# Kernel tuning notes

Hardware: AMD Instinct MI355X
Metric: run time of the kernel (lower is better)

The kernel has to match this reference:

```python
import jax, jax.numpy as jnp
import numpy as np

N_NODES = 10000
DEG = 16
E = N_NODES * DEG
IN = 256
OUT = 256
B = 2
SLOPE = 0.2


def setup_inputs() -> dict:
    key = jax.random.key(0)
    ks = jax.random.split(key, 8)
    rng = np.random.default_rng(0)
    # edges sorted by source, every node appears as a source exactly DEG times
    src = np.repeat(np.arange(N_NODES, dtype=np.int64), DEG)
    tgt = rng.integers(0, N_NODES, size=E).astype(np.int64)
    # torch.unique(..., return_inverse=True) -> sorted uniques + inverse ids
    usrc, sid = np.unique(src, return_inverse=True)
    utgt, tid = np.unique(tgt, return_inverse=True)
    s = 1.0 / np.sqrt(IN)
    sa = 1.0 / np.sqrt(2 * OUT)
    return {
        "nodes": jax.random.normal(ks[0], (N_NODES, B, IN), jnp.float32),
        "Ws": jax.random.normal(ks[1], (IN, OUT), jnp.float32) * s,
        "bs": jnp.zeros((OUT,), jnp.float32),
        "Wt": jax.random.normal(ks[2], (IN, OUT), jnp.float32) * s,
        "bt": jnp.zeros((OUT,), jnp.float32),
        "Wv": jax.random.normal(ks[3], (IN, OUT), jnp.float32) * s,
        "bv": jnp.zeros((OUT,), jnp.float32),
        "Wa": jax.random.normal(ks[4], (2 * OUT, 1), jnp.float32) * sa,
        "ba": jnp.zeros((1,), jnp.float32),
        "unique_source_node_id": jnp.asarray(usrc),
        "unique_target_node_id": jnp.asarray(utgt),
        "source_id_per_edge": jnp.asarray(sid),
        "target_id_per_edge": jnp.asarray(tid),
    }


def reference(nodes, Ws, bs, Wt, bt, Wv, bv, Wa, ba,
              unique_source_node_id, unique_target_node_id,
              source_id_per_edge, target_id_per_edge):
    Ns = unique_source_node_id.shape[0]
    # project_node_states
    src_proj = nodes[unique_source_node_id] @ Ws + bs          # [Ns, B, O]
    tgt_proj = nodes[unique_target_node_id] @ Wt + bt          # [Nt, B, O]
    # gather_node_pairs + attention + LeakyReLU
    paired = jnp.concatenate(
        [src_proj[source_id_per_edge], tgt_proj[target_id_per_edge]], axis=-1)  # [E, B, 2O]
    scores = jax.nn.leaky_relu(paired @ Wa + ba, SLOPE)        # [E, B, 1]
    # neighbourhood_softmax: exp(clip) then scatter-add over source segments
    ex = jnp.exp(jnp.clip(scores, -2.0, 2.0))
    denom = jax.ops.segment_sum(ex, source_id_per_edge, num_segments=Ns)
    alpha = ex / denom[source_id_per_edge]                     # [E, B, 1]
    # apply_attention (values_type='new')
    vals = nodes[unique_target_node_id] @ Wv + bv              # [Nt, B, O]
    weighted = alpha * vals[target_id_per_edge]                # [E, B, O]
    # aggregate_neighbours: the original indexes the per-edge weighted values
    # by target_id_per_edge along the EDGE axis (faithfully reproduced), then
    # sums contiguous same-source segments.
    gathered = weighted[target_id_per_edge]                    # [E, B, O]
    agg = jax.ops.segment_sum(gathered, source_id_per_edge, num_segments=Ns)
    # update_sources (update_type='sum'), return_only_source_nodes=True
    return src_proj + agg                                      # [Ns, B, O]
```

## Files before the change

kernel.cpp:

```cpp
#include <hip/hip_runtime.h>

#define B2 2
#define DEG 16
#define SLOPE 0.2f

typedef __attribute__((ext_vector_type(8))) short short8;
typedef __attribute__((ext_vector_type(8))) unsigned short ushort8;
typedef __attribute__((ext_vector_type(4))) unsigned short ushort4v;
typedef __attribute__((ext_vector_type(4))) float f32x4;

__device__ inline unsigned short f2bf(float f) {
  union { float f; unsigned u; } v; v.f = f;
  unsigned r = v.u + 0x7fff + ((v.u >> 16) & 1);
  return (unsigned short)(r >> 16);
}
__device__ inline float bf2f(unsigned short u) {
  union { unsigned u; float f; } c; c.u = ((unsigned)u) << 16;
  return c.f;
}
__device__ inline ushort8 f2bf8(float4 lo, float4 hi) {
  ushort8 r;
  r[0] = f2bf(lo.x); r[1] = f2bf(lo.y); r[2] = f2bf(lo.z); r[3] = f2bf(lo.w);
  r[4] = f2bf(hi.x); r[5] = f2bf(hi.y); r[6] = f2bf(hi.z); r[7] = f2bf(hi.w);
  return r;
}

__device__ inline float wave_dot256(const float* __restrict__ a,
                                    const float* __restrict__ b, int lane) {
  float4 x = *(const float4*)(a + lane * 4);
  float4 y = *(const float4*)(b + lane * 4);
  float v = x.x * y.x + x.y * y.y + x.z * y.z + x.w * y.w;
  #pragma unroll
  for (int off = 32; off; off >>= 1) v += __shfl_down(v, off);
  return v;
}

__global__ __launch_bounds__(256) void prep_w_k(
    const float* __restrict__ Ws, const float* __restrict__ Wt,
    const float* __restrict__ Wv, const float* __restrict__ Wa,
    const float* __restrict__ bs, const float* __restrict__ bt,
    unsigned short* __restrict__ WsT, unsigned short* __restrict__ WvT,
    float* __restrict__ ws_comb, float* __restrict__ wt_comb,
    float* __restrict__ consts) {
  int bx = blockIdx.x;
  if (bx < 32) {
    const float* src = (bx & 16) ? Wv : Ws;
    unsigned short* dst = (bx & 16) ? WvT : WsT;
    int rc = bx & 15;
    int r0 = (rc >> 2) * 64, c0 = (rc & 3) * 64;
    __shared__ float tile[64][65];
    int tr = threadIdx.x >> 6, tc = threadIdx.x & 63;
    #pragma unroll
    for (int i = 0; i < 16; ++i) {
      int r = tr * 16 + i;
      tile[r][tc] = src[(long)(r0 + r) * 256 + c0 + tc];
    }
    __syncthreads();
    #pragma unroll
    for (int i = 0; i < 16; ++i) {
      int r = tr * 16 + i;
      dst[(long)(c0 + r) * 256 + r0 + tc] = f2bf(tile[tc][r]);
    }
  } else {
    int wave = (bx - 32) * 4 + (threadIdx.x >> 6);
    int lane = threadIdx.x & 63;
    if (wave >= 514) return;
    const float *vec, *wa;
    float* dst;
    if (wave < 256)       { vec = Ws + (long)wave * 256;         wa = Wa;       dst = ws_comb + wave; }
    else if (wave < 512)  { vec = Wt + (long)(wave - 256) * 256; wa = Wa + 256; dst = wt_comb + (wave - 256); }
    else if (wave == 512) { vec = bs; wa = Wa;       dst = consts; }
    else                  { vec = bt; wa = Wa + 256; dst = consts + 1; }
    float v = wave_dot256(vec, wa, lane);
    if (lane == 0) *dst = v;
  }
}

__global__ __launch_bounds__(256) void logits_k(
    const float* __restrict__ nodes, const float* __restrict__ ws_comb,
    const float* __restrict__ wt_comb,
    float* __restrict__ an_s, float* __restrict__ an_t, int nrows) {
  int wave = blockIdx.x * 4 + (threadIdx.x >> 6);
  int lane = threadIdx.x & 63;
  if (wave >= nrows) return;
  const float4 a = *(const float4*)(nodes + (long)wave * 256 + lane * 4);
  const float4 w1 = *(const float4*)(ws_comb + lane * 4);
  const float4 w2 = *(const float4*)(wt_comb + lane * 4);
  float vs = a.x * w1.x + a.y * w1.y + a.z * w1.z + a.w * w1.w;
  float vt = a.x * w2.x + a.y * w2.y + a.z * w2.z + a.w * w2.w;
  #pragma unroll
  for (int off = 32; off; off >>= 1) {
    vs += __shfl_down(vs, off);
    vt += __shfl_down(vt, off);
  }
  if (lane == 0) { an_s[wave] = vs; an_t[wave] = vt; }
}

__global__ __launch_bounds__(256, 2) void gemm_mfma_k(
    const float* __restrict__ nodesf,
    const int* __restrict__ usrc, const int* __restrict__ utgt,
    const unsigned short* __restrict__ WsT, const unsigned short* __restrict__ WvT,
    const float* __restrict__ bs, const float* __restrict__ bv,
    unsigned short* __restrict__ sproj_bf, unsigned short* __restrict__ vals_bf,
    const float* __restrict__ an_s, const float* __restrict__ an_t,
    const int* __restrict__ tid_arr, const float* __restrict__ consts,
    const float* __restrict__ ba, float* __restrict__ alpha,
    int Ms, int Mt, int Ns) {
  if (blockIdx.z == 2) {
    if (blockIdx.y != 0) return;
    int g = blockIdx.x * 256 + threadIdx.x;
    int s = g >> 1, b = g & 1;
    if (s >= Ns) return;
    float base = an_s[(long)usrc[s] * B2 + b] + consts[0] + consts[1] + ba[0];
    float ex[DEG];
    float den = 0.f;
    #pragma unroll
    for (int j = 0; j < DEG; ++j) {
      int t = tid_arr[s * DEG + j];
      float sc = base + an_t[(long)utgt[t] * B2 + b];
      sc = sc > 0.f ? sc : SLOPE * sc;
      sc = fminf(2.f, fmaxf(-2.f, sc));
      float ev = __expf(sc);
      ex[j] = ev;
      den += ev;
    }
    float inv = 1.f / den;
    #pragma unroll
    for (int j = 0; j < DEG; ++j) alpha[(long)(s * DEG + j) * B2 + b] = ex[j] * inv;
    return;
  }
  bool second = blockIdx.z != 0;
  const int* idx = second ? utgt : usrc;
  const unsigned short* WT = second ? WvT : WsT;
  const float* bias = second ? bv : bs;
  unsigned short* dstC = second ? vals_bf : sproj_bf;
  int M = second ? Mt : Ms;
  int row0 = blockIdx.x * 128, col0 = blockIdx.y * 128;
  if (row0 >= M) return;

  constexpr int LDT = 72;
  __shared__ unsigned short As[128 * LDT];
  __shared__ unsigned short Bs[128 * LDT];
  int t = threadIdx.x;
  int wv = t >> 6, lane = t & 63;
  int srow = t >> 3;
  int scol = (t & 7) * 8;
  const float* ap[4];
  #pragma unroll
  for (int p = 0; p < 4; ++p) {
    int m = row0 + srow + 32 * p;
    int mc = m < M ? m : M - 1;
    long ar = (long)idx[mc >> 1] * B2 + (mc & 1);
    ap[p] = nodesf + ar * 256 + scol;
  }
  const unsigned short* bp[4];
  #pragma unroll
  for (int q = 0; q < 4; ++q)
    bp[q] = WT + (long)(col0 + srow + 32 * q) * 256 + scol;

  f32x4 acc[2][8];
  #pragma unroll
  for (int i = 0; i < 2; ++i)
    #pragma unroll
    for (int j = 0; j < 8; ++j) acc[i][j] = (f32x4)(0.f);

  float4 af[4][2];
  ushort8 bvv[4];
  #pragma unroll
  for (int p = 0; p < 4; ++p) {
    af[p][0] = *(const float4*)(ap[p]);
    af[p][1] = *(const float4*)(ap[p] + 4);
  }
  #pragma unroll
  for (int q = 0; q < 4; ++q) bvv[q] = *(const ushort8*)(bp[q]);

  #pragma unroll
  for (int k0 = 0; k0 < 256; k0 += 64) {
    __syncthreads();
    #pragma unroll
    for (int p = 0; p < 4; ++p)
      *(ushort8*)&As[(srow + 32 * p) * LDT + scol] = f2bf8(af[p][0], af[p][1]);
    #pragma unroll
    for (int q = 0; q < 4; ++q)
      *(ushort8*)&Bs[(srow + 32 * q) * LDT + scol] = bvv[q];
    __syncthreads();
    if (k0 < 192) {
      #pragma unroll
      for (int p = 0; p < 4; ++p) {
        af[p][0] = *(const float4*)(ap[p] + k0 + 64);
        af[p][1] = *(const float4*)(ap[p] + k0 + 68);
      }
      #pragma unroll
      for (int q = 0; q < 4; ++q) bvv[q] = *(const ushort8*)(bp[q] + k0 + 64);
    }
    #pragma unroll
    for (int ks = 0; ks < 64; ks += 32) {
      int ko = ks + (lane >> 4) * 8;
      short8 af0 = *(const short8*)&As[(32 * wv + (lane & 15)) * LDT + ko];
      short8 af1 = *(const short8*)&As[(32 * wv + 16 + (lane & 15)) * LDT + ko];
      #pragma unroll
      for (int j = 0; j < 8; ++j) {
        short8 bf = *(const short8*)&Bs[(16 * j + (lane & 15)) * LDT + ko];
        acc[0][j] = __builtin_amdgcn_mfma_f32_16x16x32_bf16(bf, af0, acc[0][j], 0, 0, 0);
        acc[1][j] = __builtin_amdgcn_mfma_f32_16x16x32_bf16(bf, af1, acc[1][j], 0, 0, 0);
      }
    }
  }
  int cq = lane >> 4, rl = lane & 15;
  #pragma unroll
  for (int j = 0; j < 8; ++j) {
    int col = col0 + 16 * j + 4 * cq;
    float4 b4 = *(const float4*)(bias + col);
    #pragma unroll
    for (int i = 0; i < 2; ++i) {
      int row = row0 + 32 * wv + 16 * i + rl;
      if (row < M) {
        ushort4v p;
        p[0] = f2bf(acc[i][j][0] + b4.x);
        p[1] = f2bf(acc[i][j][1] + b4.y);
        p[2] = f2bf(acc[i][j][2] + b4.z);
        p[3] = f2bf(acc[i][j][3] + b4.w);
        *(ushort4v*)(dstC + (long)row * 256 + col) = p;
      }
    }
  }
}

__global__ __launch_bounds__(256) void aggregate_k(
    const unsigned short* __restrict__ sproj, const unsigned short* __restrict__ vals,
    const float* __restrict__ alpha, const int* __restrict__ tid_arr,
    float* __restrict__ out, int Ns) {
  int s = blockIdx.x * 4 + (threadIdx.x >> 6);
  int lane = threadIdx.x & 63;
  if (s >= Ns) return;
  int f = tid_arr[s * DEG + (lane & 15)];
  int b = lane >> 5;
  float al = alpha[(long)f * B2 + b];
  int t2 = tid_arr[f];
  ushort8 sp = __builtin_nontemporal_load(
      (const ushort8*)(sproj + (long)s * 512 + lane * 8));
  float acc[8];
  #pragma unroll
  for (int k = 0; k < 8; ++k) acc[k] = bf2f(sp[k]);
  #pragma unroll
  for (int j = 0; j < DEG; ++j) {
    int rr = __shfl(t2, j);
    float aj = __shfl(al, (lane & 32) + j);
    ushort8 v = *(const ushort8*)(vals + (long)rr * 512 + lane * 8);
    #pragma unroll
    for (int k = 0; k < 8; ++k) acc[k] += aj * bf2f(v[k]);
  }
  long ob = (long)s * 512 + lane * 8;
  f32x4 p0, p1;
  p0[0] = acc[0]; p0[1] = acc[1]; p0[2] = acc[2]; p0[3] = acc[3];
  p1[0] = acc[4]; p1[1] = acc[5]; p1[2] = acc[6]; p1[3] = acc[7];
  __builtin_nontemporal_store(p0, (f32x4*)(out + ob));
  __builtin_nontemporal_store(p1, (f32x4*)(out + ob + 4));
}

extern "C" void kernel_launch(void* const* d_in, const int* in_sizes, int n_in,
                              void* d_out, int out_size, void* d_ws, size_t ws_size,
                              hipStream_t stream) {
  const float* nodes = (const float*)d_in[0];
  const float* Ws = (const float*)d_in[1];
  const float* bs = (const float*)d_in[2];
  const float* Wt = (const float*)d_in[3];
  const float* bt = (const float*)d_in[4];
  const float* Wv = (const float*)d_in[5];
  const float* bv = (const float*)d_in[6];
  const float* Wa = (const float*)d_in[7];
  const float* ba = (const float*)d_in[8];
  const int* usrc = (const int*)d_in[9];
  const int* utgt = (const int*)d_in[10];
  const int* tidp = (const int*)d_in[12];
  int Ns = in_sizes[9], Nt = in_sizes[10];
  int NsB = Ns * B2, NtB = Nt * B2;
  long nrows = in_sizes[0] / 256;

  unsigned short* WsT = (unsigned short*)d_ws;
  unsigned short* WvT = WsT + 65536;
  unsigned short* vals_bf = WvT + 65536;
  unsigned short* sproj_bf = vals_bf + (size_t)NtB * 256;
  float* fbase = (float*)(sproj_bf + (size_t)NsB * 256);
  float* an_s = fbase;
  float* an_t = an_s + nrows;
  float* ws_comb = an_t + nrows;
  float* wt_comb = ws_comb + 256;
  float* consts = wt_comb + 256;
  float* alpha = consts + 16;
  float* out = (float*)d_out;

  prep_w_k<<<161, 256, 0, stream>>>(Ws, Wt, Wv, Wa, bs, bt,
                                    WsT, WvT, ws_comb, wt_comb, consts);
  logits_k<<<(int)((nrows + 3) / 4), 256, 0, stream>>>(
      nodes, ws_comb, wt_comb, an_s, an_t, (int)nrows);
  int maxM = NsB > NtB ? NsB : NtB;
  gemm_mfma_k<<<dim3((maxM + 127) / 128, 2, 3), 256, 0, stream>>>(
      nodes, usrc, utgt, WsT, WvT, bs, bv, sproj_bf, vals_bf,
      an_s, an_t, tidp, consts, ba, alpha, NsB, NtB, Ns);
  aggregate_k<<<(Ns + 3) / 4, 256, 0, stream>>>(
      sproj_bf, vals_bf, alpha, tidp, out, Ns);
}
```

Baseline: 133.9 us.

## Fuse attention logits into GEMM A-loads and widen GEMM tile to full N

Removes the separate logits kernel by computing the per-row dot products with the combined attention vectors while the GEMM streams its A rows, reducing them with lane shuffles. The GEMM block now covers all 256 output columns, so each gathered node row is read and converted once instead of twice. Alpha computation moves into its own small kernel that runs after the GEMM, since it now depends on the GEMM's logits. This doubles the accumulator and B-tile shared memory per block, which raises register and LDS pressure and halves the grid size.

```diff
diff --git a/kernel.cpp b/kernel.cpp
--- a/kernel.cpp
+++ b/kernel.cpp
@@ -23,6 +23,10 @@
   r[0] = f2bf(lo.x); r[1] = f2bf(lo.y); r[2] = f2bf(lo.z); r[3] = f2bf(lo.w);
   r[4] = f2bf(hi.x); r[5] = f2bf(hi.y); r[6] = f2bf(hi.z); r[7] = f2bf(hi.w);
   return r;
+}
+__device__ inline float dot8(float4 a0, float4 a1, float4 c0, float4 c1) {
+  return a0.x * c0.x + a0.y * c0.y + a0.z * c0.z + a0.w * c0.w +
+         a1.x * c1.x + a1.y * c1.y + a1.z * c1.z + a1.w * c1.w;
 }
 
 __device__ inline float wave_dot256(const float* __restrict__ a,
@@ -76,71 +80,29 @@
   }
 }
 
-__global__ __launch_bounds__(256) void logits_k(
-    const float* __restrict__ nodes, const float* __restrict__ ws_comb,
-    const float* __restrict__ wt_comb,
-    float* __restrict__ an_s, float* __restrict__ an_t, int nrows) {
-  int wave = blockIdx.x * 4 + (threadIdx.x >> 6);
-  int lane = threadIdx.x & 63;
-  if (wave >= nrows) return;
-  const float4 a = *(const float4*)(nodes + (long)wave * 256 + lane * 4);
-  const float4 w1 = *(const float4*)(ws_comb + lane * 4);
-  const float4 w2 = *(const float4*)(wt_comb + lane * 4);
-  float vs = a.x * w1.x + a.y * w1.y + a.z * w1.z + a.w * w1.w;
-  float vt = a.x * w2.x + a.y * w2.y + a.z * w2.z + a.w * w2.w;
-  #pragma unroll
-  for (int off = 32; off; off >>= 1) {
-    vs += __shfl_down(vs, off);
-    vt += __shfl_down(vt, off);
-  }
-  if (lane == 0) { an_s[wave] = vs; an_t[wave] = vt; }
-}
-
 __global__ __launch_bounds__(256, 2) void gemm_mfma_k(
     const float* __restrict__ nodesf,
     const int* __restrict__ usrc, const int* __restrict__ utgt,
     const unsigned short* __restrict__ WsT, const unsigned short* __restrict__ WvT,
     const float* __restrict__ bs, const float* __restrict__ bv,
+    const float* __restrict__ ws_comb, const float* __restrict__ wt_comb,
     unsigned short* __restrict__ sproj_bf, unsigned short* __restrict__ vals_bf,
-    const float* __restrict__ an_s, const float* __restrict__ an_t,
-    const int* __restrict__ tid_arr, const float* __restrict__ consts,
-    const float* __restrict__ ba, float* __restrict__ alpha,
-    int Ms, int Mt, int Ns) {
-  if (blockIdx.z == 2) {
-    if (blockIdx.y != 0) return;
-    int g = blockIdx.x * 256 + threadIdx.x;
-    int s = g >> 1, b = g & 1;
-    if (s >= Ns) return;
-    float base = an_s[(long)usrc[s] * B2 + b] + consts[0] + consts[1] + ba[0];
-    float ex[DEG];
-    float den = 0.f;
-    #pragma unroll
-    for (int j = 0; j < DEG; ++j) {
-      int t = tid_arr[s * DEG + j];
-      float sc = base + an_t[(long)utgt[t] * B2 + b];
-      sc = sc > 0.f ? sc : SLOPE * sc;
-      sc = fminf(2.f, fmaxf(-2.f, sc));
-      float ev = __expf(sc);
-      ex[j] = ev;
-      den += ev;
-    }
-    float inv = 1.f / den;
-    #pragma unroll
-    for (int j = 0; j < DEG; ++j) alpha[(long)(s * DEG + j) * B2 + b] = ex[j] * inv;
-    return;
-  }
+    float* __restrict__ an_s_m, float* __restrict__ an_t_m,
+    int Ms, int Mt) {
   bool second = blockIdx.z != 0;
   const int* idx = second ? utgt : usrc;
   const unsigned short* WT = second ? WvT : WsT;
   const float* bias = second ? bv : bs;
+  const float* comb = second ? wt_comb : ws_comb;
   unsigned short* dstC = second ? vals_bf : sproj_bf;
+  float* anv = second ? an_t_m : an_s_m;
   int M = second ? Mt : Ms;
-  int row0 = blockIdx.x * 128, col0 = blockIdx.y * 128;
+  int row0 = blockIdx.x * 128;
   if (row0 >= M) return;
 
   constexpr int LDT = 72;
   __shared__ unsigned short As[128 * LDT];
-  __shared__ unsigned short Bs[128 * LDT];
+  __shared__ unsigned short Bs[256 * LDT];
   int t = threadIdx.x;
   int wv = t >> 6, lane = t & 63;
   int srow = t >> 3;
@@ -153,45 +115,55 @@
     long ar = (long)idx[mc >> 1] * B2 + (mc & 1);
     ap[p] = nodesf + ar * 256 + scol;
   }
-  const unsigned short* bp[4];
-  #pragma unroll
-  for (int q = 0; q < 4; ++q)
-    bp[q] = WT + (long)(col0 + srow + 32 * q) * 256 + scol;
-
-  f32x4 acc[2][8];
+  const unsigned short* bp[8];
+  #pragma unroll
+  for (int q = 0; q < 8; ++q)
+    bp[q] = WT + (long)(srow + 32 * q) * 256 + scol;
+
+  f32x4 acc[2][16];
   #pragma unroll
   for (int i = 0; i < 2; ++i)
     #pragma unroll
-    for (int j = 0; j < 8; ++j) acc[i][j] = (f32x4)(0.f);
-
-  float4 af[4][2];
-  ushort8 bvv[4];
-  #pragma unroll
-  for (int p = 0; p < 4; ++p) {
-    af[p][0] = *(const float4*)(ap[p]);
-    af[p][1] = *(const float4*)(ap[p] + 4);
-  }
-  #pragma unroll
-  for (int q = 0; q < 4; ++q) bvv[q] = *(const ushort8*)(bp[q]);
+    for (int j = 0; j < 16; ++j) acc[i][j] = (f32x4)(0.f);
+
+  ushort8 avbf[4], bvv[8];
+  float dp[4] = {0.f, 0.f, 0.f, 0.f};
+  {
+    float4 c0 = *(const float4*)(comb + scol);
+    float4 c1 = *(const float4*)(comb + scol + 4);
+    #pragma unroll
+    for (int p = 0; p < 4; ++p) {
+      float4 a0 = *(const float4*)(ap[p]);
+      float4 a1 = *(const float4*)(ap[p] + 4);
+      dp[p] += dot8(a0, a1, c0, c1);
+      avbf[p] = f2bf8(a0, a1);
+    }
+    #pragma unroll
+    for (int q = 0; q < 8; ++q) bvv[q] = *(const ushort8*)(bp[q]);
+  }
 
   #pragma unroll
   for (int k0 = 0; k0 < 256; k0 += 64) {
     __syncthreads();
     #pragma unroll
     for (int p = 0; p < 4; ++p)
-      *(ushort8*)&As[(srow + 32 * p) * LDT + scol] = f2bf8(af[p][0], af[p][1]);
-    #pragma unroll
-    for (int q = 0; q < 4; ++q)
+      *(ushort8*)&As[(srow + 32 * p) * LDT + scol] = avbf[p];
+    #pragma unroll
+    for (int q = 0; q < 8; ++q)
       *(ushort8*)&Bs[(srow + 32 * q) * LDT + scol] = bvv[q];
     __syncthreads();
     if (k0 < 192) {
+      float4 c0 = *(const float4*)(comb + k0 + 64 + scol);
+      float4 c1 = *(const float4*)(comb + k0 + 64 + scol + 4);
       #pragma unroll
       for (int p = 0; p < 4; ++p) {
-        af[p][0] = *(const float4*)(ap[p] + k0 + 64);
-        af[p][1] = *(const float4*)(ap[p] + k0 + 68);
+        float4 a0 = *(const float4*)(ap[p] + k0 + 64);
+        float4 a1 = *(const float4*)(ap[p] + k0 + 68);
+        dp[p] += dot8(a0, a1, c0, c1);
+        avbf[p] = f2bf8(a0, a1);
       }
       #pragma unroll
-      for (int q = 0; q < 4; ++q) bvv[q] = *(const ushort8*)(bp[q] + k0 + 64);
+      for (int q = 0; q < 8; ++q) bvv[q] = *(const ushort8*)(bp[q] + k0 + 64);
     }
     #pragma unroll
     for (int ks = 0; ks < 64; ks += 32) {
@@ -199,17 +171,29 @@
       short8 af0 = *(const short8*)&As[(32 * wv + (lane & 15)) * LDT + ko];
       short8 af1 = *(const short8*)&As[(32 * wv + 16 + (lane & 15)) * LDT + ko];
       #pragma unroll
-      for (int j = 0; j < 8; ++j) {
+      for (int j = 0; j < 16; ++j) {
         short8 bf = *(const short8*)&Bs[(16 * j + (lane & 15)) * LDT + ko];
         acc[0][j] = __builtin_amdgcn_mfma_f32_16x16x32_bf16(bf, af0, acc[0][j], 0, 0, 0);
         acc[1][j] = __builtin_amdgcn_mfma_f32_16x16x32_bf16(bf, af1, acc[1][j], 0, 0, 0);
       }
     }
   }
+  #pragma unroll
+  for (int mask = 1; mask <= 4; mask <<= 1) {
+    #pragma unroll
+    for (int p = 0; p < 4; ++p) dp[p] += __shfl_xor(dp[p], mask);
+  }
+  if ((t & 7) == 0) {
+    #pragma unroll
+    for (int p = 0; p < 4; ++p) {
+      int m = row0 + srow + 32 * p;
+      if (m < M) anv[m] = dp[p];
+    }
+  }
   int cq = lane >> 4, rl = lane & 15;
   #pragma unroll
-  for (int j = 0; j < 8; ++j) {
-    int col = col0 + 16 * j + 4 * cq;
+  for (int j = 0; j < 16; ++j) {
+    int col = 16 * j + 4 * cq;
     float4 b4 = *(const float4*)(bias + col);
     #pragma unroll
     for (int i = 0; i < 2; ++i) {
@@ -224,6 +208,31 @@
       }
     }
   }
+}
+
+__global__ __launch_bounds__(256) void alpha_k(
+    const float* __restrict__ an_s_m, const float* __restrict__ an_t_m,
+    const int* __restrict__ tid_arr, const float* __restrict__ consts,
+    const float* __restrict__ ba, float* __restrict__ alpha, int Ns) {
+  int g = blockIdx.x * 256 + threadIdx.x;
+  int s = g >> 1, b = g & 1;
+  if (s >= Ns) return;
+  float base = an_s_m[2 * s + b] + consts[0] + consts[1] + ba[0];
+  float ex[DEG];
+  float den = 0.f;
+  #pragma unroll
+  for (int j = 0; j < DEG; ++j) {
+    int t = tid_arr[s * DEG + j];
+    float sc = base + an_t_m[2 * t + b];
+    sc = sc > 0.f ? sc : SLOPE * sc;
+    sc = fminf(2.f, fmaxf(-2.f, sc));
+    float ev = __expf(sc);
+    ex[j] = ev;
+    den += ev;
+  }
+  float inv = 1.f / den;
+  #pragma unroll
+  for (int j = 0; j < DEG; ++j) alpha[(long)(s * DEG + j) * B2 + b] = ex[j] * inv;
 }
 
 __global__ __launch_bounds__(256) void aggregate_k(
@@ -275,16 +284,15 @@
   const int* tidp = (const int*)d_in[12];
   int Ns = in_sizes[9], Nt = in_sizes[10];
   int NsB = Ns * B2, NtB = Nt * B2;
-  long nrows = in_sizes[0] / 256;
 
   unsigned short* WsT = (unsigned short*)d_ws;
   unsigned short* WvT = WsT + 65536;
   unsigned short* vals_bf = WvT + 65536;
   unsigned short* sproj_bf = vals_bf + (size_t)NtB * 256;
   float* fbase = (float*)(sproj_bf + (size_t)NsB * 256);
-  float* an_s = fbase;
-  float* an_t = an_s + nrows;
-  float* ws_comb = an_t + nrows;
+  float* an_s_m = fbase;
+  float* an_t_m = an_s_m + NsB;
+  float* ws_comb = an_t_m + NtB;
   float* wt_comb = ws_comb + 256;
   float* consts = wt_comb + 256;
   float* alpha = consts + 16;
@@ -292,12 +300,12 @@
 
   prep_w_k<<<161, 256, 0, stream>>>(Ws, Wt, Wv, Wa, bs, bt,
                                     WsT, WvT, ws_comb, wt_comb, consts);
-  logits_k<<<(int)((nrows + 3) / 4), 256, 0, stream>>>(
-      nodes, ws_comb, wt_comb, an_s, an_t, (int)nrows);
   int maxM = NsB > NtB ? NsB : NtB;
-  gemm_mfma_k<<<dim3((maxM + 127) / 128, 2, 3), 256, 0, stream>>>(
-      nodes, usrc, utgt, WsT, WvT, bs, bv, sproj_bf, vals_bf,
-      an_s, an_t, tidp, consts, ba, alpha, NsB, NtB, Ns);
+  gemm_mfma_k<<<dim3((maxM + 127) / 128, 1, 2), 256, 0, stream>>>(
+      nodes, usrc, utgt, WsT, WvT, bs, bv, ws_comb, wt_comb,
+      sproj_bf, vals_bf, an_s_m, an_t_m, NsB, NtB);
+  alpha_k<<<(NsB + 255) / 256, 256, 0, stream>>>(
+      an_s_m, an_t_m, tidp, consts, ba, alpha, Ns);
   aggregate_k<<<(Ns + 3) / 4, 256, 0, stream>>>(
       sproj_bf, vals_bf, alpha, tidp, out, Ns);
 }
```

New measurement: 146.5 us. 1.09x slower.
